# Kernel optimization log

Hardware: AMD Instinct MI355X
Metric: run time of the kernel (lower is better)

## Reference

```python
import jax, jax.numpy as jnp
import numpy as np

MARGIN = 1.0  # init kwarg 'margin'
N, D = 8192, 128
NUM_CLASSES = 100

def setup_inputs() -> dict:
    key = jax.random.key(0)
    kx, ky = jax.random.split(key)
    x = jax.random.normal(kx, (N, D), dtype=jnp.float32)
    y = jax.random.randint(ky, (N,), 0, NUM_CLASSES, dtype=jnp.int64)
    return {"x": x, "y": y}

def reference(x, y):
    # Squared euclidean pairwise distances: d[i,j] = sum_k (x[i,k] - x[j,k])^2
    # computed via the ||a||^2 + ||b||^2 - 2 a.b expansion to avoid an NxNxD
    # intermediate. Clamp tiny negatives from fp roundoff.
    sq = jnp.sum(x * x, axis=-1)                      # [N]
    d = sq[:, None] + sq[None, :] - 2.0 * (x @ x.T)   # [N, N]
    d = jnp.maximum(d, 0.0)
    same = (y[:, None] == y[None, :]).astype(x.dtype)  # [N, N] positive-pair mask
    # Faithful to the torch module: dissimilar pairs contribute d, similar
    # pairs contribute hinge clamp(margin - d, 0); mean over all N*N pairs.
    loss = jnp.mean((1.0 - same) * d + same * jnp.maximum(MARGIN - d, 0.0))
    return loss
```

## Files before the change

kernel.cpp:

```cpp
#include <hip/hip_runtime.h>


#define N_ROWS 8192
#define DIM    128
#define NCLS   100
#define CAP    224
#define RB     32
#define SCB    1024
#define GBPC   8
#define GRAMB  (NCLS * GBPC)
#define NREP   8

typedef _Float16 half8  __attribute__((ext_vector_type(8)));
typedef _Float16 half4v __attribute__((ext_vector_type(4)));
typedef float    float4v __attribute__((ext_vector_type(4)));

__global__ __launch_bounds__(256) void rank_kernel(
    const int* __restrict__ y, int* __restrict__ cnt, int* __restrict__ rank)
{
    const int tid = threadIdx.x, r = blockIdx.x * 256 + tid;
    __shared__ int lcnt[NCLS], lbase[NCLS];
    if (tid < NCLS) lcnt[tid] = 0;
    __syncthreads();
    const int c = y[r];
    const int intra = atomicAdd(&lcnt[c], 1);
    __syncthreads();
    if (tid < NCLS && lcnt[tid] > 0)
        lbase[tid] = atomicAdd(&cnt[tid], lcnt[tid]);
    __syncthreads();
    rank[r] = lbase[c] + intra;
}

__global__ __launch_bounds__(256) void scan_kernel(
    const float* __restrict__ x, const int* __restrict__ y,
    const int* __restrict__ rank,
    _Float16* __restrict__ gh, float* __restrict__ sqg,
    float* __restrict__ Scol8, float* __restrict__ SQc8)
{
    const int b = blockIdx.x, tid = threadIdx.x;
    const int l = tid & 31, g = tid >> 5;
    const int r = b * 8 + g;
    const int rep = b & (NREP - 1);
    const float4* x4 = (const float4*)x;
    __shared__ float4 colred[256];

    float4 v = x4[r * 32 + l];
    float s = v.x*v.x + v.y*v.y + v.z*v.z + v.w*v.w;
    s += __shfl_xor(s, 1);  s += __shfl_xor(s, 2);  s += __shfl_xor(s, 4);
    s += __shfl_xor(s, 8);  s += __shfl_xor(s, 16);
    const int c = y[r];
    const int p = rank[r];
    if (p < CAP) {
        half4v h;
        h[0] = (_Float16)v.x; h[1] = (_Float16)v.y;
        h[2] = (_Float16)v.z; h[3] = (_Float16)v.w;
        *(half4v*)(gh + (size_t)(c * CAP + p) * DIM + l * 4) = h;
        if (l == 0) sqg[c * CAP + p] = s;
    }
    if (l == 0) atomicAdd(&SQc8[rep * NCLS + c], s);

    colred[tid] = v;
    __syncthreads();
    if (tid < 32) {
        float4 a = colred[tid];
        #pragma unroll
        for (int gg = 1; gg < 8; ++gg) {
            float4 t = colred[tid + 32 * gg];
            a.x += t.x; a.y += t.y; a.z += t.z; a.w += t.w;
        }
        float* dst = Scol8 + rep * DIM;
        atomicAdd(&dst[4 * tid + 0], a.x);
        atomicAdd(&dst[4 * tid + 1], a.y);
        atomicAdd(&dst[4 * tid + 2], a.z);
        atomicAdd(&dst[4 * tid + 3], a.w);
    }
}

__global__ __launch_bounds__(256) void gram_kernel(
    const _Float16* __restrict__ gh, const float* __restrict__ sqg,
    const int* __restrict__ cnt,
    const float* __restrict__ Scol8, const float* __restrict__ SQc8,
    float* __restrict__ Hsum, float* __restrict__ SSsum,
    int* __restrict__ done, float* __restrict__ out)
{
    const int c = blockIdx.x >> 3, qq = blockIdx.x & 7, tid = threadIdx.x;
    __shared__ float wred[8];
    __shared__ int   lastFlag;

    const int mtrue = cnt[c];
    const int m = mtrue < CAP ? mtrue : CAP;
    const int ntiles = (m + 15) >> 4;
    const int ntp = ntiles * (ntiles + 1) / 2;

    const int wave = tid >> 6, lane = tid & 63;
    const int lr = lane & 15, q = lane >> 4;
    float hacc = 0.f, dsum = 0.f;
    const _Float16* base = gh + (size_t)c * CAP * DIM;
    const float* sqb_ = sqg + c * CAP;

    for (int tp = qq * 4 + wave; tp < ntp; tp += 32) {
        int ta = 0, rem = tp;
        while (rem >= ntiles - ta) { rem -= ntiles - ta; ++ta; }
        const int tb = ta + rem;
        const half8* ap = (const half8*)(base + (ta * 16 + lr) * DIM + q * 8);
        const half8* bp = (const half8*)(base + (tb * 16 + lr) * DIM + q * 8);
        float4v acc = {0.f, 0.f, 0.f, 0.f};
        #pragma unroll
        for (int kb = 0; kb < 4; ++kb)
            acc = __builtin_amdgcn_mfma_f32_16x16x32_f16(ap[kb * 4], bp[kb * 4], acc, 0, 0, 0);
        const float w = (ta == tb) ? 1.f : 2.f;
        const int bb = tb * 16 + lr;
        const float sqb = (bb < m) ? sqb_[bb] : 0.f;
        #pragma unroll
        for (int i = 0; i < 4; ++i) {
            const int a = ta * 16 + q * 4 + i;
            if (a < m && bb < m) {
                const float dot = acc[i];
                dsum += w * dot;
                if (a != bb) {
                    float d = fmaxf(sqb_[a] + sqb - 2.f * dot, 0.f);
                    hacc += w * fmaxf(1.f - d, 0.f);
                }
            }
        }
    }
    #pragma unroll
    for (int off = 32; off > 0; off >>= 1) {
        hacc += __shfl_xor(hacc, off);
        dsum += __shfl_xor(dsum, off);
    }
    if (lane == 0) { wred[wave] = hacc; wred[4 + wave] = dsum; }
    __syncthreads();
    if (tid == 0) {
        float h = wred[0] + wred[1] + wred[2] + wred[3];
        float d = wred[4] + wred[5] + wred[6] + wred[7];
        if (h != 0.f) atomicAdd(Hsum, h);
        if (d != 0.f) atomicAdd(SSsum, d);
        __threadfence();
        int p = atomicAdd(done, 1);
        lastFlag = (p == GRAMB - 1);
    }
    __syncthreads();
    if (!lastFlag) return;

    __threadfence();
    const double Nf = (double)N_ROWS;
    double contrib = 0.0;
    if (tid < DIM) {
        float sc = 0.f;
        #pragma unroll
        for (int k = 0; k < NREP; ++k) sc += Scol8[k * DIM + tid];
        contrib -= 2.0 * (double)sc * (double)sc;
    }
    if (tid < NCLS) {
        float qv = 0.f;
        #pragma unroll
        for (int k = 0; k < NREP; ++k) qv += SQc8[k * NCLS + tid];
        contrib += 2.0 * (double)qv * (Nf - (double)cnt[tid]);
    }
    if (tid == 0) {
        float H  = __hip_atomic_load(Hsum,  __ATOMIC_RELAXED, __HIP_MEMORY_SCOPE_AGENT);
        float SS = __hip_atomic_load(SSsum, __ATOMIC_RELAXED, __HIP_MEMORY_SCOPE_AGENT);
        contrib += 2.0 * (double)SS + (double)H + Nf * 1.0 ;
    }
    __shared__ double dred[256];
    dred[tid] = contrib;
    __syncthreads();
    for (int s = 128; s > 0; s >>= 1) {
        if (tid < s) dred[tid] += dred[tid + s];
        __syncthreads();
    }
    if (tid == 0) out[0] = (float)(dred[0] / (Nf * Nf));
}

extern "C" void kernel_launch(void* const* d_in, const int* in_sizes, int n_in,
                              void* d_out, int out_size, void* d_ws, size_t ws_size,
                              hipStream_t stream) {
    const float* x = (const float*)d_in[0];
    const int*   y = (const int*)d_in[1];

    _Float16* gh = (_Float16*)d_ws;
    float* sqg   = (float*)(gh + (size_t)NCLS * CAP * DIM);
    int*   rank  = (int*)(sqg + NCLS * CAP);
    float* Scol8 = (float*)(rank + N_ROWS);
    float* SQc8  = Scol8 + NREP * DIM;
    float* Hsum  = SQc8 + NREP * NCLS;
    float* SSsum = Hsum + 1;
    int*   cnt   = (int*)(SSsum + 1);
    int*   done  = cnt + NCLS;
    const size_t zero_words = NREP * DIM + NREP * NCLS + 2 + NCLS + 1;

    hipMemsetAsync(Scol8, 0, zero_words * sizeof(float), stream);
    rank_kernel<<<RB,    256, 0, stream>>>(y, cnt, rank);
    scan_kernel<<<SCB,   256, 0, stream>>>(x, y, rank, gh, sqg, Scol8, SQc8);
    gram_kernel<<<GRAMB, 256, 0, stream>>>(gh, sqg, cnt, Scol8, SQc8,
                                           Hsum, SSsum, done, (float*)d_out);
}
```

Measured before the change: 98.17 us.

## Fuse rank, scan and gram kernels into one cooperative grid-synced kernel

Merges the three launches into a single cooperative kernel that computes class slots with per-row global atomics, scatters fp16 rows, and then runs the per-class Gram pass after a grid-wide sync. The separate rank kernel goes away, replaced by one atomicAdd per row on the class counter. This is meant to remove launch gaps and intermediate kernel boundaries. In exchange it adds a grid barrier with 1024 co-resident blocks and more contention on the class-count atomics.

```diff
diff --git a/kernel.cpp b/kernel.cpp
--- a/kernel.cpp
+++ b/kernel.cpp
@@ -1,12 +1,14 @@
 #include <hip/hip_runtime.h>
+#include <hip/hip_cooperative_groups.h>
+
+namespace cg = cooperative_groups;
 
 
 #define N_ROWS 8192
 #define DIM    128
 #define NCLS   100
 #define CAP    224
-#define RB     32
-#define SCB    1024
+#define NBLK   1024
 #define GBPC   8
 #define GRAMB  (NCLS * GBPC)
 #define NREP   8
@@ -15,78 +17,66 @@
 typedef _Float16 half4v __attribute__((ext_vector_type(4)));
 typedef float    float4v __attribute__((ext_vector_type(4)));
 
-__global__ __launch_bounds__(256) void rank_kernel(
-    const int* __restrict__ y, int* __restrict__ cnt, int* __restrict__ rank)
-{
-    const int tid = threadIdx.x, r = blockIdx.x * 256 + tid;
-    __shared__ int lcnt[NCLS], lbase[NCLS];
-    if (tid < NCLS) lcnt[tid] = 0;
-    __syncthreads();
-    const int c = y[r];
-    const int intra = atomicAdd(&lcnt[c], 1);
-    __syncthreads();
-    if (tid < NCLS && lcnt[tid] > 0)
-        lbase[tid] = atomicAdd(&cnt[tid], lcnt[tid]);
-    __syncthreads();
-    rank[r] = lbase[c] + intra;
-}
-
-__global__ __launch_bounds__(256) void scan_kernel(
+__global__ __launch_bounds__(256, 4) void fused_kernel(
     const float* __restrict__ x, const int* __restrict__ y,
-    const int* __restrict__ rank,
     _Float16* __restrict__ gh, float* __restrict__ sqg,
-    float* __restrict__ Scol8, float* __restrict__ SQc8)
-{
-    const int b = blockIdx.x, tid = threadIdx.x;
-    const int l = tid & 31, g = tid >> 5;
-    const int r = b * 8 + g;
-    const int rep = b & (NREP - 1);
-    const float4* x4 = (const float4*)x;
-    __shared__ float4 colred[256];
-
-    float4 v = x4[r * 32 + l];
-    float s = v.x*v.x + v.y*v.y + v.z*v.z + v.w*v.w;
-    s += __shfl_xor(s, 1);  s += __shfl_xor(s, 2);  s += __shfl_xor(s, 4);
-    s += __shfl_xor(s, 8);  s += __shfl_xor(s, 16);
-    const int c = y[r];
-    const int p = rank[r];
-    if (p < CAP) {
-        half4v h;
-        h[0] = (_Float16)v.x; h[1] = (_Float16)v.y;
-        h[2] = (_Float16)v.z; h[3] = (_Float16)v.w;
-        *(half4v*)(gh + (size_t)(c * CAP + p) * DIM + l * 4) = h;
-        if (l == 0) sqg[c * CAP + p] = s;
-    }
-    if (l == 0) atomicAdd(&SQc8[rep * NCLS + c], s);
-
-    colred[tid] = v;
-    __syncthreads();
-    if (tid < 32) {
-        float4 a = colred[tid];
-        #pragma unroll
-        for (int gg = 1; gg < 8; ++gg) {
-            float4 t = colred[tid + 32 * gg];
-            a.x += t.x; a.y += t.y; a.z += t.z; a.w += t.w;
-        }
-        float* dst = Scol8 + rep * DIM;
-        atomicAdd(&dst[4 * tid + 0], a.x);
-        atomicAdd(&dst[4 * tid + 1], a.y);
-        atomicAdd(&dst[4 * tid + 2], a.z);
-        atomicAdd(&dst[4 * tid + 3], a.w);
-    }
-}
-
-__global__ __launch_bounds__(256) void gram_kernel(
-    const _Float16* __restrict__ gh, const float* __restrict__ sqg,
-    const int* __restrict__ cnt,
-    const float* __restrict__ Scol8, const float* __restrict__ SQc8,
+    int* __restrict__ cnt,
+    float* __restrict__ Scol8, float* __restrict__ SQc8,
     float* __restrict__ Hsum, float* __restrict__ SSsum,
     int* __restrict__ done, float* __restrict__ out)
 {
-    const int c = blockIdx.x >> 3, qq = blockIdx.x & 7, tid = threadIdx.x;
+    const int b = blockIdx.x, tid = threadIdx.x;
+    __shared__ float4 colred[256];
+
+    {
+        const int l = tid & 31, g = tid >> 5;
+        const int r = b * 8 + g;
+        const int rep = b & (NREP - 1);
+        const float4* x4 = (const float4*)x;
+
+        float4 v = x4[r * 32 + l];
+        float s = v.x*v.x + v.y*v.y + v.z*v.z + v.w*v.w;
+        s += __shfl_xor(s, 1);  s += __shfl_xor(s, 2);  s += __shfl_xor(s, 4);
+        s += __shfl_xor(s, 8);  s += __shfl_xor(s, 16);
+        const int c = y[r];
+        int p = 0;
+        if (l == 0) p = atomicAdd(&cnt[c], 1);
+        p = __shfl(p, tid & 32);
+        if (p < CAP) {
+            half4v h;
+            h[0] = (_Float16)v.x; h[1] = (_Float16)v.y;
+            h[2] = (_Float16)v.z; h[3] = (_Float16)v.w;
+            *(half4v*)(gh + (size_t)(c * CAP + p) * DIM + l * 4) = h;
+            if (l == 0) sqg[c * CAP + p] = s;
+        }
+        if (l == 0) atomicAdd(&SQc8[rep * NCLS + c], s);
+
+        colred[tid] = v;
+        __syncthreads();
+        if (tid < 32) {
+            float4 a = colred[tid];
+            #pragma unroll
+            for (int gg = 1; gg < 8; ++gg) {
+                float4 t = colred[tid + 32 * gg];
+                a.x += t.x; a.y += t.y; a.z += t.z; a.w += t.w;
+            }
+            float* dst = Scol8 + rep * DIM;
+            atomicAdd(&dst[4 * tid + 0], a.x);
+            atomicAdd(&dst[4 * tid + 1], a.y);
+            atomicAdd(&dst[4 * tid + 2], a.z);
+            atomicAdd(&dst[4 * tid + 3], a.w);
+        }
+    }
+
+    __threadfence();
+    cg::this_grid().sync();
+
+    if (b >= GRAMB) return;
+
     __shared__ float wred[8];
     __shared__ int   lastFlag;
 
+    const int c = b >> 3, qq = b & 7;
     const int mtrue = cnt[c];
     const int m = mtrue < CAP ? mtrue : CAP;
     const int ntiles = (m + 15) >> 4;
@@ -181,8 +171,7 @@
 
     _Float16* gh = (_Float16*)d_ws;
     float* sqg   = (float*)(gh + (size_t)NCLS * CAP * DIM);
-    int*   rank  = (int*)(sqg + NCLS * CAP);
-    float* Scol8 = (float*)(rank + N_ROWS);
+    float* Scol8 = (float*)(sqg + NCLS * CAP);
     float* SQc8  = Scol8 + NREP * DIM;
     float* Hsum  = SQc8 + NREP * NCLS;
     float* SSsum = Hsum + 1;
@@ -190,9 +179,12 @@
     int*   done  = cnt + NCLS;
     const size_t zero_words = NREP * DIM + NREP * NCLS + 2 + NCLS + 1;
 
+    float* outp = (float*)d_out;
+
     hipMemsetAsync(Scol8, 0, zero_words * sizeof(float), stream);
-    rank_kernel<<<RB,    256, 0, stream>>>(y, cnt, rank);
-    scan_kernel<<<SCB,   256, 0, stream>>>(x, y, rank, gh, sqg, Scol8, SQc8);
-    gram_kernel<<<GRAMB, 256, 0, stream>>>(gh, sqg, cnt, Scol8, SQc8,
-                                           Hsum, SSsum, done, (float*)d_out);
+    void* args[] = { (void*)&x, (void*)&y, (void*)&gh, (void*)&sqg, (void*)&cnt,
+                     (void*)&Scol8, (void*)&SQc8, (void*)&Hsum, (void*)&SSsum,
+                     (void*)&done, (void*)&outp };
+    hipLaunchCooperativeKernel((const void*)fused_kernel, dim3(NBLK), dim3(256),
+                               args, 0, stream);
 }
```

Result: slower. 243.1 us (+147.6%).
